# Kernel optimization log

Measured on AMD Instinct MI355X. Metric: run time of the kernel, lower is better.

## Reference

```python
import jax, jax.numpy as jnp
import numpy as np

D_IN = 1024
D_OUT = 1024
NUM_HEADS = 16
HEAD_DIM = D_OUT // NUM_HEADS


def setup_inputs() -> dict:
    key = jax.random.key(0)
    ks = jax.random.split(key, 6)
    s = 0.02
    x = jax.random.normal(ks[0], (1, 4096, D_IN), dtype=jnp.float32)
    W_q = jax.random.normal(ks[1], (D_IN, D_OUT), dtype=jnp.float32) * s
    W_k = jax.random.normal(ks[2], (D_IN, D_OUT), dtype=jnp.float32) * s
    W_v = jax.random.normal(ks[3], (D_IN, D_OUT), dtype=jnp.float32) * s
    W_o = jax.random.normal(ks[4], (D_OUT, D_OUT), dtype=jnp.float32) * s
    b_o = jnp.zeros((D_OUT,), dtype=jnp.float32)
    return {"x": x, "W_q": W_q, "W_k": W_k, "W_v": W_v, "W_o": W_o, "b_o": b_o}


def reference(x, W_q, W_k, W_v, W_o, b_o):
    b, n, _ = x.shape
    # project and split heads: [b, h, n, d]
    def split_heads(t):
        return t.reshape(b, n, NUM_HEADS, HEAD_DIM).transpose(0, 2, 1, 3)
    q = split_heads(x @ W_q)
    k = split_heads(x @ W_k)
    v = split_heads(x @ W_v)
    scale = 1.0 / jnp.sqrt(jnp.float32(HEAD_DIM))
    scores = jnp.einsum('bhqd,bhkd->bhqk', q, k) * scale  # [b,h,n,n]
    causal = jnp.tril(jnp.ones((n, n), dtype=bool))
    scores = jnp.where(causal, scores, -jnp.inf)
    weights = jax.nn.softmax(scores, axis=-1)
    # dropout rate is 0.0 -> identity
    ctx = jnp.einsum('bhqk,bhkd->bhqd', weights, v)
    ctx = ctx.transpose(0, 2, 1, 3).reshape(b, n, D_OUT)
    return ctx @ W_o + b_o
```

## Files before the change

### kernel.cpp

```cpp
#include <hip/hip_runtime.h>
#include <hip/hip_bf16.h>

typedef __hip_bfloat16 bf16;
typedef __attribute__((ext_vector_type(8))) short short8;
typedef __attribute__((ext_vector_type(4))) float floatx4;

#define SEQ 4096
#define DIM 1024
#define NH 16
#define HD 64

#if defined(__has_builtin)
#if __has_builtin(__builtin_amdgcn_exp2f)
#define EXP2(x) __builtin_amdgcn_exp2f(x)
#endif
#endif
#ifndef EXP2
#define EXP2(x) exp2f(x)
#endif

__device__ __forceinline__ short f2s(float f) { bf16 t = __float2bfloat16(f); return *(short*)&t; }

__device__ __forceinline__ void gload16(const void* g, void* l) {
    __builtin_amdgcn_global_load_lds(
        (const __attribute__((address_space(1))) void*)g,
        (__attribute__((address_space(3))) void*)l, 16, 0, 0);
}

__device__ __forceinline__ short8 cvt8(float4 a, float4 b) {
    short8 s;
    s[0] = f2s(a.x); s[1] = f2s(a.y); s[2] = f2s(a.z); s[3] = f2s(a.w);
    s[4] = f2s(b.x); s[5] = f2s(b.y); s[6] = f2s(b.z); s[7] = f2s(b.w);
    return s;
}

__global__ __launch_bounds__(256) void transpose_cast_kernel(
    const float* __restrict__ W0, const float* __restrict__ W1,
    const float* __restrict__ W2, const float* __restrict__ W3,
    bf16* __restrict__ Wt_all)
{
    const float* W = blockIdx.z == 0 ? W0 : blockIdx.z == 1 ? W1
                   : blockIdx.z == 2 ? W2 : W3;
    bf16* Wt = Wt_all + (size_t)blockIdx.z * DIM * DIM;

    __shared__ float tile[32][33];
    const int n0 = blockIdx.x * 32, k0 = blockIdx.y * 32;
    const int tr = threadIdx.x >> 5;
    const int tc = threadIdx.x & 31;
#pragma unroll
    for (int i = 0; i < 32; i += 8)
        tile[tr + i][tc] = W[(size_t)(k0 + tr + i) * DIM + n0 + tc];
    __syncthreads();
#pragma unroll
    for (int i = 0; i < 32; i += 8)
        Wt[(size_t)(n0 + tr + i) * DIM + k0 + tc] = __float2bfloat16(tile[tc][tr + i]);
}

#define QBM 128
#define QBN 128
#define QBK 64

__global__ __launch_bounds__(256) void qkv_gemm_kernel(
    const float* __restrict__ A, const bf16* __restrict__ Wt,
    bf16* __restrict__ Qb, bf16* __restrict__ Kb, bf16* __restrict__ Vb)
{
    const int z = blockIdx.z;
    const bf16* Bt = Wt + (size_t)z * DIM * DIM;
    bf16* C = z == 0 ? Qb : (z == 1 ? Kb : Vb);
    const float osc = (z == 0) ? 0.18033688f : 1.0f;

    __shared__ alignas(16) float Af[QBM][QBK];
    __shared__ alignas(16) short Bs[QBN][QBK];

    const int tid  = threadIdx.x;
    const int wave = tid >> 6, lane = tid & 63;
    const int l15  = lane & 15, quad = lane >> 4;
    const int wm = (wave & 1) * 64;
    const int wn = (wave >> 1) * 64;
    const int bm = blockIdx.y * QBM;
    const int bn = blockIdx.x * QBN;

    const int arow = tid >> 4;
    const int agch = (tid & 15) ^ (arow & 15);
    const float* gA = A + (size_t)(bm + arow) * DIM + agch * 4;
    char* ldsA = (char*)&Af[0][0] + wave * 1024;

    const int brow = tid >> 3;
    const int bgch = (tid & 7) ^ (brow & 7);
    const bf16* gB = Bt + (size_t)(bn + brow) * DIM + bgch * 8;
    char* ldsB = (char*)&Bs[0][0] + wave * 1024;

    floatx4 acc[4][4] = {};

    for (int k0 = 0; k0 < DIM; k0 += QBK) {
        __syncthreads();
#pragma unroll
        for (int c = 0; c < 8; ++c)
            gload16(gA + (size_t)c * 16 * DIM + k0, ldsA + c * 4096);
#pragma unroll
        for (int c = 0; c < 4; ++c)
            gload16(gB + (size_t)c * 32 * DIM + k0, ldsB + c * 4096);
        __syncthreads();

#pragma unroll
        for (int c2 = 0; c2 < 2; ++c2) {
            const int g0 = c2 * 8 + quad * 2;
            const int cb = (c2 * 4 + quad) ^ (l15 & 7);
            short8 afr[4], bfr[4];
#pragma unroll
            for (int i = 0; i < 4; ++i) {
                const int ra = wm + i * 16 + l15;
                float4 f0 = *(const float4*)&Af[ra][(g0 ^ l15) * 4];
                float4 f1 = *(const float4*)&Af[ra][((g0 + 1) ^ l15) * 4];
                afr[i] = cvt8(f0, f1);
                bfr[i] = *(const short8*)&Bs[wn + i * 16 + l15][cb * 8];
            }
#pragma unroll
            for (int mi = 0; mi < 4; ++mi)
#pragma unroll
                for (int ni = 0; ni < 4; ++ni)
                    acc[mi][ni] = __builtin_amdgcn_mfma_f32_16x16x32_bf16(
                        afr[mi], bfr[ni], acc[mi][ni], 0, 0, 0);
        }
    }

#pragma unroll
    for (int mi = 0; mi < 4; ++mi)
#pragma unroll
        for (int r = 0; r < 4; ++r) {
            const int row = bm + wm + mi * 16 + quad * 4 + r;
#pragma unroll
            for (int ni = 0; ni < 4; ++ni) {
                const int col = bn + wn + ni * 16 + l15;
                C[(size_t)row * DIM + col] = __float2bfloat16(acc[mi][ni][r] * osc);
            }
        }
}

__global__ __launch_bounds__(256) void out_gemm_kernel(
    const bf16* __restrict__ A, const bf16* __restrict__ Bt,
    const float* __restrict__ bias, float* __restrict__ C)
{
    __shared__ alignas(16) short Asl[128][64];
    __shared__ alignas(16) short Bsl[64][64];

    const int tid  = threadIdx.x;
    const int wave = tid >> 6, lane = tid & 63;
    const int l15  = lane & 15, quad = lane >> 4;
    const int wm = (wave & 1) * 64;
    const int wn = (wave >> 1) * 32;
    const int bm = blockIdx.y * 128;
    const int bn = blockIdx.x * 64;

    const int srow   = tid >> 3;
    const int gchunk = (tid & 7) ^ (srow & 7);
    const bf16* gA = A  + (size_t)(bm + srow) * DIM + gchunk * 8;
    const bf16* gB = Bt + (size_t)(bn + srow) * DIM + gchunk * 8;
    char* ldsA = (char*)&Asl[0][0] + wave * 1024;
    char* ldsB = (char*)&Bsl[0][0] + wave * 1024;

    floatx4 acc[4][2] = {};

    for (int k0 = 0; k0 < DIM; k0 += 64) {
        __syncthreads();
#pragma unroll
        for (int c = 0; c < 4; ++c)
            gload16(gA + (size_t)c * 32 * DIM + k0, ldsA + c * 4096);
#pragma unroll
        for (int c = 0; c < 2; ++c)
            gload16(gB + (size_t)c * 32 * DIM + k0, ldsB + c * 4096);
        __syncthreads();

#pragma unroll
        for (int c2 = 0; c2 < 2; ++c2) {
            const int cb = (c2 * 4 + quad) ^ (l15 & 7);
            short8 afr[4], bfr[2];
#pragma unroll
            for (int i = 0; i < 4; ++i)
                afr[i] = *(const short8*)&Asl[wm + i * 16 + l15][cb * 8];
#pragma unroll
            for (int i = 0; i < 2; ++i)
                bfr[i] = *(const short8*)&Bsl[wn + i * 16 + l15][cb * 8];
#pragma unroll
            for (int mi = 0; mi < 4; ++mi)
#pragma unroll
                for (int ni = 0; ni < 2; ++ni)
                    acc[mi][ni] = __builtin_amdgcn_mfma_f32_16x16x32_bf16(
                        afr[mi], bfr[ni], acc[mi][ni], 0, 0, 0);
        }
    }

#pragma unroll
    for (int mi = 0; mi < 4; ++mi)
#pragma unroll
        for (int r = 0; r < 4; ++r) {
            const int row = bm + wm + mi * 16 + quad * 4 + r;
#pragma unroll
            for (int ni = 0; ni < 2; ++ni) {
                const int col = bn + wn + ni * 16 + l15;
                C[(size_t)row * DIM + col] = acc[mi][ni][r] + bias[col];
            }
        }
}

#define QT 128
#define KT 64
#define LDT 72

__global__ __launch_bounds__(256) void flash_attn_kernel(
    const bf16* __restrict__ Q, const bf16* __restrict__ K,
    const bf16* __restrict__ V, bf16* ctx)
{
    const int lin  = blockIdx.y * 32 + blockIdx.x;
    const int half = lin >> 8, idx = lin & 255;
    const int qj   = half ? (idx & 31) : 31 - (idx & 31);
    const int h    = (idx >> 5) + 8 * half;
    const int q0   = qj * QT;
    const int nkt  = 2 * qj + 2;

    const int tid  = threadIdx.x;
    const int wave = tid >> 6;
    const int lane = tid & 63;
    const int l15  = lane & 15;
    const int quad = lane >> 4;

    __shared__ alignas(16) short Ks[2][KT][LDT];
    __shared__ alignas(16) short Vt[2][HD][LDT];

    short8 qfrag[2][2];
#pragma unroll
    for (int s = 0; s < 2; ++s) {
        const bf16* qp = Q + (size_t)(q0 + wave * 32 + s * 16 + l15) * DIM
                       + h * HD + quad * 8;
#pragma unroll
        for (int c = 0; c < 2; ++c)
            qfrag[s][c] = *(const short8*)(qp + c * 32);
    }

    const int kr = tid >> 2, kc = (tid & 3) * 16;
    const int vr = (tid & 31) * 2, vd = (tid >> 5) * 8;
    const int vslot = ((vr >> 5) & 1) * 32 + ((vr >> 2) & 3) * 8
                    + ((vr >> 4) & 1) * 4  + ((vr >> 1) & 1) * 2;

    short8 kreg0, kreg1, vreg0, vreg1;
    {
        const short8* kp  = (const short8*)(K + (size_t)kr * DIM + h * HD + kc);
        kreg0 = kp[0]; kreg1 = kp[1];
        const short8* vp0 = (const short8*)(V + (size_t)vr * DIM + h * HD + vd);
        const short8* vp1 = (const short8*)(V + (size_t)(vr + 1) * DIM + h * HD + vd);
        vreg0 = vp0[0]; vreg1 = vp1[0];
    }
    *(short8*)&Ks[0][kr][kc]     = kreg0;
    *(short8*)&Ks[0][kr][kc + 8] = kreg1;
#pragma unroll
    for (int i = 0; i < 8; ++i) {
        unsigned int pv = (unsigned int)(unsigned short)vreg0[i]
                        | ((unsigned int)(unsigned short)vreg1[i] << 16);
        *(unsigned int*)&Vt[0][vd + i][vslot] = pv;
    }
    {
        const size_t nb = (size_t)KT;
        const short8* kp  = (const short8*)(K + (nb + kr) * DIM + h * HD + kc);
        kreg0 = kp[0]; kreg1 = kp[1];
        const short8* vp0 = (const short8*)(V + (nb + vr) * DIM + h * HD + vd);
        const short8* vp1 = (const short8*)(V + (nb + vr + 1) * DIM + h * HD + vd);
        vreg0 = vp0[0]; vreg1 = vp1[0];
    }

    __syncthreads();

    short8 onesf;
#pragma unroll
    for (int i = 0; i < 8; ++i) onesf[i] = (short)0x3F80;

    floatx4 o_acc[2][4] = {};
    floatx4 lacc[2] = {};

    for (int kt = 0; kt < nkt; ++kt) {
        const int b = kt & 1;

        floatx4 sT[2][4] = {};
#pragma unroll
        for (int n = 0; n < 4; ++n)
#pragma unroll
            for (int c = 0; c < 2; ++c) {
                short8 kf = *(const short8*)&Ks[b][n * 16 + l15][c * 32 + quad * 8];
#pragma unroll
                for (int s = 0; s < 2; ++s)
                    sT[s][n] = __builtin_amdgcn_mfma_f32_16x16x32_bf16(
                        kf, qfrag[s][c], sT[s][n], 0, 0, 0);
            }

        if (kt + 1 < nkt) {
            *(short8*)&Ks[b ^ 1][kr][kc]     = kreg0;
            *(short8*)&Ks[b ^ 1][kr][kc + 8] = kreg1;
#pragma unroll
            for (int i = 0; i < 8; ++i) {
                unsigned int pv = (unsigned int)(unsigned short)vreg0[i]
                                | ((unsigned int)(unsigned short)vreg1[i] << 16);
                *(unsigned int*)&Vt[b ^ 1][vd + i][vslot] = pv;
            }
            if (kt + 2 < nkt) {
                const size_t nb = (size_t)(kt + 2) * KT;
                const short8* kp  = (const short8*)(K + (nb + kr) * DIM + h * HD + kc);
                kreg0 = kp[0]; kreg1 = kp[1];
                const short8* vp0 = (const short8*)(V + (nb + vr) * DIM + h * HD + vd);
                const short8* vp1 = (const short8*)(V + (nb + vr + 1) * DIM + h * HD + vd);
                vreg0 = vp0[0]; vreg1 = vp1[0];
            }
        }

        short8 pfrag[2][2];
        const int kbase = kt * KT;
        if (kt >= nkt - 2) {
#pragma unroll
            for (int s = 0; s < 2; ++s) {
                const int qrow = q0 + wave * 32 + s * 16 + l15;
                float p[4][4];
#pragma unroll
                for (int n = 0; n < 4; ++n) {
                    const int key0 = kbase + n * 16 + quad * 4;
#pragma unroll
                    for (int r = 0; r < 4; ++r)
                        p[n][r] = (key0 + r <= qrow) ? EXP2(sT[s][n][r]) : 0.f;
                }
#pragma unroll
                for (int c = 0; c < 2; ++c) {
                    short8 f;
#pragma unroll
                    for (int j = 0; j < 8; ++j)
                        f[j] = f2s(p[c * 2 + (j >> 2)][j & 3]);
                    pfrag[s][c] = f;
                }
            }
        } else {
#pragma unroll
            for (int s = 0; s < 2; ++s)
#pragma unroll
                for (int c = 0; c < 2; ++c) {
                    short8 f;
#pragma unroll
                    for (int j = 0; j < 8; ++j)
                        f[j] = f2s(EXP2(sT[s][c * 2 + (j >> 2)][j & 3]));
                    pfrag[s][c] = f;
                }
        }

#pragma unroll
        for (int n = 0; n < 4; ++n)
#pragma unroll
            for (int c = 0; c < 2; ++c) {
                short8 vf = *(const short8*)&Vt[b][n * 16 + l15][c * 32 + quad * 8];
#pragma unroll
                for (int s = 0; s < 2; ++s)
                    o_acc[s][n] = __builtin_amdgcn_mfma_f32_16x16x32_bf16(
                        pfrag[s][c], vf, o_acc[s][n], 0, 0, 0);
            }
#pragma unroll
        for (int s = 0; s < 2; ++s) {
            lacc[s] = __builtin_amdgcn_mfma_f32_16x16x32_bf16(pfrag[s][0], onesf, lacc[s], 0, 0, 0);
            lacc[s] = __builtin_amdgcn_mfma_f32_16x16x32_bf16(pfrag[s][1], onesf, lacc[s], 0, 0, 0);
        }

        __syncthreads();
    }

#pragma unroll
    for (int s = 0; s < 2; ++s)
#pragma unroll
        for (int r = 0; r < 4; ++r) {
            const float inv = 1.0f / lacc[s][r];
            const int row = q0 + wave * 32 + s * 16 + quad * 4 + r;
#pragma unroll
            for (int n = 0; n < 4; ++n)
                ctx[(size_t)row * DIM + h * HD + n * 16 + l15] =
                    __float2bfloat16(o_acc[s][n][r] * inv);
        }
}

extern "C" void kernel_launch(void* const* d_in, const int* in_sizes, int n_in,
                              void* d_out, int out_size, void* d_ws, size_t ws_size,
                              hipStream_t stream)
{
    const float* x  = (const float*)d_in[0];
    const float* Wq = (const float*)d_in[1];
    const float* Wk = (const float*)d_in[2];
    const float* Wv = (const float*)d_in[3];
    const float* Wo = (const float*)d_in[4];
    const float* bo = (const float*)d_in[5];
    float* out = (float*)d_out;

    bf16* Wt_all = (bf16*)d_ws;
    bf16* Qb     = Wt_all + (size_t)4 * DIM * DIM;
    bf16* V      = (bf16*)d_out;
    bf16* Kb     = V + (size_t)SEQ * DIM;
    bf16* ctx    = Qb;
    const bf16* Wot = Wt_all + (size_t)3 * DIM * DIM;

    transpose_cast_kernel<<<dim3(32, 32, 4), 256, 0, stream>>>(Wq, Wk, Wv, Wo, Wt_all);

    qkv_gemm_kernel<<<dim3(DIM / QBN, SEQ / QBM, 3), 256, 0, stream>>>(
        x, Wt_all, Qb, Kb, V);

    flash_attn_kernel<<<dim3(32, NH), 256, 0, stream>>>(Qb, Kb, V, ctx);

    out_gemm_kernel<<<dim3(DIM / 64, SEQ / 128), 256, 0, stream>>>(
        ctx, Wot, bo, out);
}
```

Baseline: 193.2 us.

## Double KV tile to 128, load K via direct-to-LDS DMA with XOR swizzle

Raises the attention key tile from 64 to 128 rows, which halves the number of loop iterations and barriers per query tile. K is now staged with global_load_lds DMA straight into a swizzled, unpadded LDS layout instead of going through registers, and the loads for the next tile are issued before the QK MFMAs. V is still loaded through registers, transposed, and written with an XOR swizzle that replaces the padding. The larger tiles raise register pressure (sT has 16 floatx4 values, pfrag has 8 fragments) and use more LDS, which may lower occupancy. The causal diagonal tile also does more masked work than before.

```diff
diff --git a/kernel.cpp b/kernel.cpp
--- a/kernel.cpp
+++ b/kernel.cpp
@@ -204,8 +204,7 @@
 }
 
 #define QT 128
-#define KT 64
-#define LDT 72
+#define KT 128
 
 __global__ __launch_bounds__(256) void flash_attn_kernel(
     const bf16* __restrict__ Q, const bf16* __restrict__ K,
@@ -216,7 +215,7 @@
     const int qj   = half ? (idx & 31) : 31 - (idx & 31);
     const int h    = (idx >> 5) + 8 * half;
     const int q0   = qj * QT;
-    const int nkt  = 2 * qj + 2;
+    const int nkt  = qj + 1;
 
     const int tid  = threadIdx.x;
     const int wave = tid >> 6;
@@ -224,8 +223,8 @@
     const int l15  = lane & 15;
     const int quad = lane >> 4;
 
-    __shared__ alignas(16) short Ks[2][KT][LDT];
-    __shared__ alignas(16) short Vt[2][HD][LDT];
+    __shared__ alignas(16) short Ks[2][KT][HD];
+    __shared__ alignas(16) short Vt[2][HD][KT];
 
     short8 qfrag[2][2];
 #pragma unroll
@@ -237,36 +236,47 @@
             qfrag[s][c] = *(const short8*)(qp + c * 32);
     }
 
-    const int kr = tid >> 2, kc = (tid & 3) * 16;
-    const int vr = (tid & 31) * 2, vd = (tid >> 5) * 8;
-    const int vslot = ((vr >> 5) & 1) * 32 + ((vr >> 2) & 3) * 8
-                    + ((vr >> 4) & 1) * 4  + ((vr >> 1) & 1) * 2;
-
-    short8 kreg0, kreg1, vreg0, vreg1;
-    {
-        const short8* kp  = (const short8*)(K + (size_t)kr * DIM + h * HD + kc);
-        kreg0 = kp[0]; kreg1 = kp[1];
-        const short8* vp0 = (const short8*)(V + (size_t)vr * DIM + h * HD + vd);
-        const short8* vp1 = (const short8*)(V + (size_t)(vr + 1) * DIM + h * HD + vd);
-        vreg0 = vp0[0]; vreg1 = vp1[0];
-    }
-    *(short8*)&Ks[0][kr][kc]     = kreg0;
-    *(short8*)&Ks[0][kr][kc + 8] = kreg1;
-#pragma unroll
-    for (int i = 0; i < 8; ++i) {
-        unsigned int pv = (unsigned int)(unsigned short)vreg0[i]
-                        | ((unsigned int)(unsigned short)vreg1[i] << 16);
-        *(unsigned int*)&Vt[0][vd + i][vslot] = pv;
-    }
-    {
-        const size_t nb = (size_t)KT;
-        const short8* kp  = (const short8*)(K + (nb + kr) * DIM + h * HD + kc);
-        kreg0 = kp[0]; kreg1 = kp[1];
-        const short8* vp0 = (const short8*)(V + (nb + vr) * DIM + h * HD + vd);
-        const short8* vp1 = (const short8*)(V + (nb + vr + 1) * DIM + h * HD + vd);
-        vreg0 = vp0[0]; vreg1 = vp1[0];
-    }
-
+    const int krow8 = wave * 8 + (lane >> 3);
+    const int kgch  = (lane & 7) ^ ((lane >> 3) & 7);
+
+#define STAGE_K_DMA(kb, buf) do {                                             \
+    char* _dst = (char*)&Ks[buf][0][0] + wave * 1024;                         \
+    const bf16* _src = K + (size_t)((kb) + krow8) * DIM + h * HD + kgch * 8;  \
+    _Pragma("unroll")                                                         \
+    for (int _c = 0; _c < 4; ++_c)                                            \
+        gload16(_src + (size_t)_c * 32 * DIM, _dst + _c * 4096);              \
+} while (0)
+
+    const int vr = (tid & 63) * 2, vd = (tid >> 6) * 8;
+    const int vslot = (vr & 0x63) | ((vr & 0x0C) << 1) | ((vr & 0x10) >> 2);
+    const int vch0  = vslot >> 3, vo = vslot & 7;
+
+    short8 vreg0, vreg0b, vreg1, vreg1b;
+
+#define LOAD_V(kb) do {                                                       \
+    const bf16* _vb = V + (size_t)((kb) + vr) * DIM + h * HD + vd;            \
+    vreg0  = *(const short8*)(_vb);                                           \
+    vreg0b = *(const short8*)(_vb + 32);                                      \
+    vreg1  = *(const short8*)(_vb + DIM);                                     \
+    vreg1b = *(const short8*)(_vb + DIM + 32);                                \
+} while (0)
+
+#define STAGE_V(buf) do {                                                     \
+    _Pragma("unroll")                                                         \
+    for (int _i = 0; _i < 8; ++_i) {                                          \
+        const int _s = ((vch0 ^ ((vd + _i) & 7)) << 3) + vo;                  \
+        unsigned int _lo = (unsigned int)(unsigned short)vreg0[_i]            \
+                         | ((unsigned int)(unsigned short)vreg1[_i] << 16);   \
+        unsigned int _hi = (unsigned int)(unsigned short)vreg0b[_i]           \
+                         | ((unsigned int)(unsigned short)vreg1b[_i] << 16);  \
+        *(unsigned int*)&Vt[buf][vd + _i][_s] = _lo;                          \
+        *(unsigned int*)&Vt[buf][vd + 32 + _i][_s] = _hi;                     \
+    }                                                                         \
+} while (0)
+
+    STAGE_K_DMA(0, 0);
+    LOAD_V(0);
+    STAGE_V(0);
     __syncthreads();
 
     short8 onesf;
@@ -279,53 +289,42 @@
     for (int kt = 0; kt < nkt; ++kt) {
         const int b = kt & 1;
 
-        floatx4 sT[2][4] = {};
-#pragma unroll
-        for (int n = 0; n < 4; ++n)
+        if (kt + 1 < nkt) {
+            STAGE_K_DMA((size_t)(kt + 1) * KT, b ^ 1);
+            LOAD_V((size_t)(kt + 1) * KT);
+        }
+
+        floatx4 sT[2][8] = {};
+#pragma unroll
+        for (int n = 0; n < 8; ++n)
 #pragma unroll
             for (int c = 0; c < 2; ++c) {
-                short8 kf = *(const short8*)&Ks[b][n * 16 + l15][c * 32 + quad * 8];
+                short8 kf = *(const short8*)
+                    &Ks[b][n * 16 + l15][(((c * 4 + quad) ^ (l15 & 7))) * 8];
 #pragma unroll
                 for (int s = 0; s < 2; ++s)
                     sT[s][n] = __builtin_amdgcn_mfma_f32_16x16x32_bf16(
                         kf, qfrag[s][c], sT[s][n], 0, 0, 0);
             }
 
-        if (kt + 1 < nkt) {
-            *(short8*)&Ks[b ^ 1][kr][kc]     = kreg0;
-            *(short8*)&Ks[b ^ 1][kr][kc + 8] = kreg1;
-#pragma unroll
-            for (int i = 0; i < 8; ++i) {
-                unsigned int pv = (unsigned int)(unsigned short)vreg0[i]
-                                | ((unsigned int)(unsigned short)vreg1[i] << 16);
-                *(unsigned int*)&Vt[b ^ 1][vd + i][vslot] = pv;
-            }
-            if (kt + 2 < nkt) {
-                const size_t nb = (size_t)(kt + 2) * KT;
-                const short8* kp  = (const short8*)(K + (nb + kr) * DIM + h * HD + kc);
-                kreg0 = kp[0]; kreg1 = kp[1];
-                const short8* vp0 = (const short8*)(V + (nb + vr) * DIM + h * HD + vd);
-                const short8* vp1 = (const short8*)(V + (nb + vr + 1) * DIM + h * HD + vd);
-                vreg0 = vp0[0]; vreg1 = vp1[0];
-            }
-        }
-
-        short8 pfrag[2][2];
-        const int kbase = kt * KT;
-        if (kt >= nkt - 2) {
+        if (kt + 1 < nkt) STAGE_V(b ^ 1);
+
+        short8 pfrag[2][4];
+        if (kt == nkt - 1) {
+            const int kbase = kt * KT;
 #pragma unroll
             for (int s = 0; s < 2; ++s) {
                 const int qrow = q0 + wave * 32 + s * 16 + l15;
-                float p[4][4];
-#pragma unroll
-                for (int n = 0; n < 4; ++n) {
+                float p[8][4];
+#pragma unroll
+                for (int n = 0; n < 8; ++n) {
                     const int key0 = kbase + n * 16 + quad * 4;
 #pragma unroll
                     for (int r = 0; r < 4; ++r)
                         p[n][r] = (key0 + r <= qrow) ? EXP2(sT[s][n][r]) : 0.f;
                 }
 #pragma unroll
-                for (int c = 0; c < 2; ++c) {
+                for (int c = 0; c < 4; ++c) {
                     short8 f;
 #pragma unroll
                     for (int j = 0; j < 8; ++j)
@@ -337,7 +336,7 @@
 #pragma unroll
             for (int s = 0; s < 2; ++s)
 #pragma unroll
-                for (int c = 0; c < 2; ++c) {
+                for (int c = 0; c < 4; ++c) {
                     short8 f;
 #pragma unroll
                     for (int j = 0; j < 8; ++j)
@@ -349,18 +348,20 @@
 #pragma unroll
         for (int n = 0; n < 4; ++n)
 #pragma unroll
-            for (int c = 0; c < 2; ++c) {
-                short8 vf = *(const short8*)&Vt[b][n * 16 + l15][c * 32 + quad * 8];
+            for (int c = 0; c < 4; ++c) {
+                short8 vf = *(const short8*)
+                    &Vt[b][n * 16 + l15][(((c * 4 + quad) ^ (l15 & 7))) * 8];
 #pragma unroll
                 for (int s = 0; s < 2; ++s)
                     o_acc[s][n] = __builtin_amdgcn_mfma_f32_16x16x32_bf16(
                         pfrag[s][c], vf, o_acc[s][n], 0, 0, 0);
             }
 #pragma unroll
-        for (int s = 0; s < 2; ++s) {
-            lacc[s] = __builtin_amdgcn_mfma_f32_16x16x32_bf16(pfrag[s][0], onesf, lacc[s], 0, 0, 0);
-            lacc[s] = __builtin_amdgcn_mfma_f32_16x16x32_bf16(pfrag[s][1], onesf, lacc[s], 0, 0, 0);
-        }
+        for (int s = 0; s < 2; ++s)
+#pragma unroll
+            for (int c = 0; c < 4; ++c)
+                lacc[s] = __builtin_amdgcn_mfma_f32_16x16x32_bf16(
+                    pfrag[s][c], onesf, lacc[s], 0, 0, 0);
 
         __syncthreads();
     }
@@ -376,6 +377,9 @@
                 ctx[(size_t)row * DIM + h * HD + n * 16 + l15] =
                     __float2bfloat16(o_acc[s][n][r] * inv);
         }
+#undef STAGE_K_DMA
+#undef LOAD_V
+#undef STAGE_V
 }
 
 extern "C" void kernel_launch(void* const* d_in, const int* in_sizes, int n_in,
```

New measurement: 288.4 us. 1.49x slower.

## Register-prefetch fp32 A tiles and convert once to bf16 LDS in QKV GEMM

Applied to the files above, without the earlier changes.

In the QKV projection GEMM, A tiles are now prefetched into registers one K-step ahead, converted to bf16 once per element and stored into a swizzled bf16 LDS tile. Previously fp32 A was copied straight to LDS and every wave reconverted it on each fragment read. This halves A's LDS footprint and read traffic and removes the redundant conversions, at the cost of more VGPRs for the prefetch buffer. Some __syncthreads in the attention kernel are also replaced by a barrier that waits only on lgkmcnt, which avoids draining outstanding global loads at those points.

```diff
diff --git a/kernel.cpp b/kernel.cpp
--- a/kernel.cpp
+++ b/kernel.cpp
@@ -3,6 +3,7 @@
 
 typedef __hip_bfloat16 bf16;
 typedef __attribute__((ext_vector_type(8))) short short8;
+typedef __attribute__((ext_vector_type(4))) short short4v;
 typedef __attribute__((ext_vector_type(4))) float floatx4;
 
 #define SEQ 4096
@@ -27,6 +28,11 @@
         (__attribute__((address_space(3))) void*)l, 16, 0, 0);
 }
 
+__device__ __forceinline__ void barrier_lgkm() {
+    asm volatile("s_waitcnt lgkmcnt(0)" ::: "memory");
+    __builtin_amdgcn_s_barrier();
+}
+
 __device__ __forceinline__ short8 cvt8(float4 a, float4 b) {
     short8 s;
     s[0] = f2s(a.x); s[1] = f2s(a.y); s[2] = f2s(a.z); s[3] = f2s(a.w);
@@ -69,7 +75,7 @@
     bf16* C = z == 0 ? Qb : (z == 1 ? Kb : Vb);
     const float osc = (z == 0) ? 0.18033688f : 1.0f;
 
-    __shared__ alignas(16) float Af[QBM][QBK];
+    __shared__ alignas(16) short As[QBM][QBK];
     __shared__ alignas(16) short Bs[QBN][QBK];
 
     const int tid  = threadIdx.x;
@@ -80,39 +86,48 @@
     const int bm = blockIdx.y * QBM;
     const int bn = blockIdx.x * QBN;
 
-    const int arow = tid >> 4;
-    const int agch = (tid & 15) ^ (arow & 15);
-    const float* gA = A + (size_t)(bm + arow) * DIM + agch * 4;
-    char* ldsA = (char*)&Af[0][0] + wave * 1024;
+    const int ar = tid >> 1, ac = (tid & 1) * 32;
+    const float* gA = A + (size_t)(bm + ar) * DIM + ac;
 
     const int brow = tid >> 3;
     const int bgch = (tid & 7) ^ (brow & 7);
     const bf16* gB = Bt + (size_t)(bn + brow) * DIM + bgch * 8;
     char* ldsB = (char*)&Bs[0][0] + wave * 1024;
 
+    float4 areg[8];
+#define LOAD_A(k0) do {                                                       \
+    _Pragma("unroll")                                                         \
+    for (int _i = 0; _i < 8; ++_i)                                            \
+        areg[_i] = *(const float4*)(gA + (k0) + _i * 4);                      \
+} while (0)
+
+#define STAGE_A() do {                                                        \
+    _Pragma("unroll")                                                         \
+    for (int _i = 0; _i < 4; ++_i) {                                          \
+        const int _ch = ((ac >> 3) + _i) ^ (ar & 7);                          \
+        *(short8*)&As[ar][_ch * 8] = cvt8(areg[2 * _i], areg[2 * _i + 1]);    \
+    }                                                                         \
+} while (0)
+
     floatx4 acc[4][4] = {};
 
+    LOAD_A(0);
     for (int k0 = 0; k0 < DIM; k0 += QBK) {
-        __syncthreads();
-#pragma unroll
-        for (int c = 0; c < 8; ++c)
-            gload16(gA + (size_t)c * 16 * DIM + k0, ldsA + c * 4096);
+        barrier_lgkm();
+        STAGE_A();
 #pragma unroll
         for (int c = 0; c < 4; ++c)
             gload16(gB + (size_t)c * 32 * DIM + k0, ldsB + c * 4096);
         __syncthreads();
+        if (k0 + QBK < DIM) LOAD_A(k0 + QBK);
 
 #pragma unroll
         for (int c2 = 0; c2 < 2; ++c2) {
-            const int g0 = c2 * 8 + quad * 2;
             const int cb = (c2 * 4 + quad) ^ (l15 & 7);
             short8 afr[4], bfr[4];
 #pragma unroll
             for (int i = 0; i < 4; ++i) {
-                const int ra = wm + i * 16 + l15;
-                float4 f0 = *(const float4*)&Af[ra][(g0 ^ l15) * 4];
-                float4 f1 = *(const float4*)&Af[ra][((g0 + 1) ^ l15) * 4];
-                afr[i] = cvt8(f0, f1);
+                afr[i] = *(const short8*)&As[wm + i * 16 + l15][cb * 8];
                 bfr[i] = *(const short8*)&Bs[wn + i * 16 + l15][cb * 8];
             }
 #pragma unroll
@@ -135,6 +150,8 @@
                 C[(size_t)row * DIM + col] = __float2bfloat16(acc[mi][ni][r] * osc);
             }
         }
+#undef LOAD_A
+#undef STAGE_A
 }
 
 __global__ __launch_bounds__(256) void out_gemm_kernel(
@@ -267,7 +284,7 @@
         vreg0 = vp0[0]; vreg1 = vp1[0];
     }
 
-    __syncthreads();
+    barrier_lgkm();
 
     short8 onesf;
 #pragma unroll
@@ -362,7 +379,7 @@
             lacc[s] = __builtin_amdgcn_mfma_f32_16x16x32_bf16(pfrag[s][1], onesf, lacc[s], 0, 0, 0);
         }
 
-        __syncthreads();
+        barrier_lgkm();
     }
 
 #pragma unroll
```

Result: slower. 231.3 us (+19.8%).
